# Performance work log

Hardware: AMD Instinct MI355X
Metric: run time of the kernel (lower is better)

The kernel has to match this reference:

```python
import jax, jax.numpy as jnp
import numpy as np

D_INNER = 1024
STATE = 16
DT_RANK = 64  # ceil(d_inner / 16)
LOG_EPS = -7.0
CLAMP = 20.0


def setup_inputs() -> dict:
    key = jax.random.key(0)
    ks = jax.random.split(key, 4)
    B, L = 2, 1024
    x = jax.random.normal(ks[0], (B, L, D_INNER), jnp.float32)
    # x_proj: Linear(d_inner -> dt_rank + 2*state_size, bias=False); stored as (in, out)
    W_xproj = jax.random.normal(ks[1], (D_INNER, DT_RANK + 2 * STATE), jnp.float32) * 0.02
    # dt_proj: Linear(dt_rank -> d_inner, bias=True)
    W_dt = jax.random.normal(ks[2], (DT_RANK, D_INNER), jnp.float32) * 0.02
    b_dt = jax.random.normal(ks[3], (D_INNER,), jnp.float32) * 0.02
    # A_log = log(arange(1..state_size)) repeated over d_inner rows
    A_log = jnp.log(jnp.tile(jnp.arange(1, STATE + 1, dtype=jnp.float32), (D_INNER, 1)))
    D = jnp.ones((D_INNER,), jnp.float32)
    return {"x": x, "W_xproj": W_xproj, "W_dt": W_dt, "b_dt": b_dt, "A_log": A_log, "D": D}


def reference(x, W_xproj, W_dt, b_dt, A_log, D):
    # x: (B, L, d_inner)
    proj = x @ W_xproj  # (B, L, dt_rank + 2*N)
    dt_inter = proj[..., :DT_RANK]
    B_ssm = proj[..., DT_RANK:DT_RANK + STATE]   # (B, L, N)
    C_ssm = proj[..., DT_RANK + STATE:]          # (B, L, N)

    delta = jax.nn.softplus(dt_inter @ W_dt + b_dt)  # (B, L, d_inner)

    # discretization (ZOH)
    A = -jnp.exp(A_log)  # (d_inner, N), negative
    log_delta_A = jnp.clip(delta[..., None] * A[None, None], LOG_EPS, CLAMP)
    delta_A = jnp.exp(log_delta_A)                              # (B, L, d, N)
    delta_B_u = (delta[..., None] * B_ssm[:, :, None, :]) * x[..., None]  # (B, L, d, N)

    # log-space cumsum scan
    log_dA = jnp.log(jnp.clip(delta_A, 1e-7, None))
    log_R = jnp.cumsum(log_dA, axis=1)
    R = jnp.exp(jnp.minimum(log_R, CLAMP))
    exp_neg_log_R = jnp.exp(jnp.minimum(-log_R, CLAMP))
    S = jnp.cumsum(delta_B_u * exp_neg_log_R, axis=1)
    h = R * S  # (B, L, d, N)

    y = jnp.einsum('bln,bldn->bld', C_ssm, h) + x * D
    return y
```

## Files before the change

kernel.cpp:

```cpp
#include <hip/hip_runtime.h>
#include <math.h>

#define D_INNER 1024
#define STATE   16
#define DT_RANK 64
#define NPROJ   96
#define LSEQ    1024
#define NBATCH  2

#define LOG2E   1.4426950408889634f
#define NEG7L2  (-7.0f * LOG2E)
#define P20L2   (20.0f * LOG2E)

template<int CTRL, int RMASK>
__device__ __forceinline__ float dppadd(float v) {
    int t = __builtin_amdgcn_update_dpp(0, __float_as_int(v), CTRL, RMASK, 0xf, false);
    return v + __int_as_float(t);
}
__device__ __forceinline__ float wave_iscan(float v) {
    v = dppadd<0x111, 0xf>(v);
    v = dppadd<0x112, 0xf>(v);
    v = dppadd<0x114, 0xf>(v);
    v = dppadd<0x118, 0xf>(v);
    v = dppadd<0x142, 0xa>(v);
    v = dppadd<0x143, 0xc>(v);
    return v;
}

__global__ __launch_bounds__(768) void proj_kernel(
        const float* __restrict__ x, const float* __restrict__ Wx,
        float* __restrict__ projdt, float* __restrict__ Bg, float* __restrict__ Cg) {
    const int tid = threadIdx.x;
    const int j  = tid % 96;
    const int kq = tid / 96;
    const int row0 = blockIdx.x * 8;

    __shared__ float xs[8 * 1024];
    __shared__ float red[8][8][96];

    {
        const float4* src = (const float4*)(x + (size_t)row0 * 1024);
        #pragma unroll
        for (int i = 0; i < 3; ++i) {
            int idx = tid + 768 * i;
            if (idx < 2048) {
                float4 v = src[idx];
                *(float4*)&xs[idx * 4] = v;
            }
        }
    }
    __syncthreads();

    const float* wp = Wx + (size_t)(kq * 128) * 96 + j;
    const float* xk = &xs[kq * 128];

    float a[8];
    #pragma unroll
    for (int r = 0; r < 8; ++r) a[r] = 0.f;

    #pragma unroll 8
    for (int k = 0; k < 128; ++k) {
        float w = wp[(size_t)k * 96];
        #pragma unroll
        for (int r = 0; r < 8; ++r)
            a[r] = fmaf(xk[r * 1024 + k], w, a[r]);
    }

    #pragma unroll
    for (int r = 0; r < 8; ++r) red[kq][r][j] = a[r];
    __syncthreads();

    {
        const int r  = tid / 96;
        const int jj = tid % 96;
        float s = 0.f;
        #pragma unroll
        for (int p = 0; p < 8; ++p) s += red[p][r][jj];
        const int row = row0 + r;
        const int b = row >> 10, l = row & 1023;
        if (jj < 64)      projdt[(size_t)row * 64 + jj] = s;
        else if (jj < 80) Bg[((size_t)b * 16 + (jj - 64)) * 1024 + l] = s;
        else              Cg[((size_t)b * 16 + (jj - 80)) * 1024 + l] = s;
    }
}

__global__ __launch_bounds__(256) void delta_kernel(
        const float* __restrict__ projdt, const float* __restrict__ Wdt,
        const float* __restrict__ bdt, const float* __restrict__ x,
        float* __restrict__ delta_t, float* __restrict__ u_t) {
    const int bid = blockIdx.x;
    const int lt = bid >> 4;
    const int dt = bid & 15;
    const int row0 = lt * 64;
    const int d0 = dt * 64;
    const int tid = threadIdx.x;

    __shared__ float pl[64][69];
    __shared__ float wlbuf[64 * 68];
    __shared__ float dtile[64][65];
    float (*wl)[68] = (float(*)[68])wlbuf;

    {
        const float4* src = (const float4*)(projdt + (size_t)row0 * 64);
        #pragma unroll
        for (int i = 0; i < 4; ++i) {
            int f4i = tid + 256 * i;
            float4 v = src[f4i];
            int l = f4i >> 4, k4 = (f4i & 15) << 2;
            pl[l][k4+0] = v.x; pl[l][k4+1] = v.y; pl[l][k4+2] = v.z; pl[l][k4+3] = v.w;
        }
    }
    {
        #pragma unroll
        for (int i = 0; i < 4; ++i) {
            int f4i = tid + 256 * i;
            int k = f4i >> 4, m4 = (f4i & 15) << 2;
            float4 v = *(const float4*)(Wdt + (size_t)k * 1024 + d0 + m4);
            *(float4*)&wl[k][m4] = v;
        }
    }
    __syncthreads();

    const int lsub = tid & 63;
    const int dq = tid >> 6;
    float acc[16];
    #pragma unroll
    for (int i = 0; i < 16; ++i) acc[i] = 0.f;

    #pragma unroll 4
    for (int k = 0; k < 64; ++k) {
        float p = pl[lsub][k];
        const float4* wr = (const float4*)&wl[k][dq * 16];
        float4 w0 = wr[0], w1 = wr[1], w2 = wr[2], w3 = wr[3];
        acc[0]  = fmaf(p, w0.x, acc[0]);  acc[1]  = fmaf(p, w0.y, acc[1]);
        acc[2]  = fmaf(p, w0.z, acc[2]);  acc[3]  = fmaf(p, w0.w, acc[3]);
        acc[4]  = fmaf(p, w1.x, acc[4]);  acc[5]  = fmaf(p, w1.y, acc[5]);
        acc[6]  = fmaf(p, w1.z, acc[6]);  acc[7]  = fmaf(p, w1.w, acc[7]);
        acc[8]  = fmaf(p, w2.x, acc[8]);  acc[9]  = fmaf(p, w2.y, acc[9]);
        acc[10] = fmaf(p, w2.z, acc[10]); acc[11] = fmaf(p, w2.w, acc[11]);
        acc[12] = fmaf(p, w3.x, acc[12]); acc[13] = fmaf(p, w3.y, acc[13]);
        acc[14] = fmaf(p, w3.z, acc[14]); acc[15] = fmaf(p, w3.w, acc[15]);
    }

    #pragma unroll
    for (int i = 0; i < 16; ++i) {
        float v = acc[i] + bdt[d0 + dq * 16 + i];
        float sp = fmaxf(v, 0.f) + log1pf(__expf(-fabsf(v)));
        dtile[dq * 16 + i][lsub] = sp;
    }
    __syncthreads();

    float (*xs)[65] = (float(*)[65])wlbuf;
    {
        #pragma unroll
        for (int i = 0; i < 4; ++i) {
            int f4i = tid + 256 * i;
            int l = f4i >> 4, m4 = (f4i & 15) << 2;
            float4 v = *(const float4*)(x + (size_t)(row0 + l) * 1024 + d0 + m4);
            xs[l][m4+0] = v.x; xs[l][m4+1] = v.y; xs[l][m4+2] = v.z; xs[l][m4+3] = v.w;
        }
    }
    __syncthreads();

    {
        int dp_ = tid >> 2, seg = tid & 3;
        int b = row0 >> 10, l0 = row0 & 1023;
        size_t off = ((size_t)b * 1024 + d0 + dp_) * 1024 + l0 + seg * 16;
        float* ddst = delta_t + off;
        float* udst = u_t + off;
        #pragma unroll
        for (int m = 0; m < 4; ++m) {
            int lb = seg * 16 + m * 4;
            float4 v;
            v.x = dtile[dp_][lb + 0];
            v.y = dtile[dp_][lb + 1];
            v.z = dtile[dp_][lb + 2];
            v.w = dtile[dp_][lb + 3];
            float4 u;
            u.x = v.x * xs[lb + 0][dp_];
            u.y = v.y * xs[lb + 1][dp_];
            u.z = v.z * xs[lb + 2][dp_];
            u.w = v.w * xs[lb + 3][dp_];
            ((float4*)ddst)[m] = v;
            ((float4*)udst)[m] = u;
        }
    }
}

__global__ __launch_bounds__(256, 6) void scan_kernel(
        float* delta_m,
        const float* __restrict__ u_t,
        const float* __restrict__ Bg, const float* __restrict__ Cg,
        const float* __restrict__ A_log, const float* __restrict__ Dvec) {
    const int bid0 = blockIdx.x;
    const int bid  = (bid0 & 7) * 256 + (bid0 >> 3);
    const int b = bid >> 10;
    const int d = bid & 1023;
    const int lane = threadIdx.x & 63;
    const int q = threadIdx.x >> 6;
    const int l0 = q * 256 + lane * 4;

    __shared__ float tot1[4][4];
    __shared__ float tot2[4][4];

    const size_t choff = ((size_t)b * 1024 + d) * 1024 + l0;
    const float4 d4 = *(const float4*)(delta_m + choff);
    const float4 u4 = *(const float4*)(u_t + choff);
    const float* Bp = Bg + (size_t)b * 16 * 1024 + l0;
    const float* Cp = Cg + (size_t)b * 16 * 1024 + l0;

    const float Dd = Dvec[d];
    float y0 = u4.x * __builtin_amdgcn_rcpf(d4.x) * Dd;
    float y1 = u4.y * __builtin_amdgcn_rcpf(d4.y) * Dd;
    float y2 = u4.z * __builtin_amdgcn_rcpf(d4.z) * Dd;
    float y3 = u4.w * __builtin_amdgcn_rcpf(d4.w) * Dd;

    #pragma unroll 1
    for (int g = 0; g < 4; ++g) {
        float A2[4], coff[4];
        #pragma unroll
        for (int j = 0; j < 4; ++j)
            A2[j] = -__expf(A_log[d * 16 + g * 4 + j]) * LOG2E;

        #pragma unroll
        for (int j = 0; j < 4; ++j) {
            float a = A2[j];
            float local = fmaxf(d4.x * a, NEG7L2) + fmaxf(d4.y * a, NEG7L2)
                        + fmaxf(d4.z * a, NEG7L2) + fmaxf(d4.w * a, NEG7L2);
            float incl = wave_iscan(local);
            if (lane == 63) tot1[j][q] = incl;
            coff[j] = incl - local;
        }
        __syncthreads();
        #pragma unroll
        for (int j = 0; j < 4; ++j) {
            float4 t = *(const float4*)&tot1[j][0];
            float w = 0.f;
            w += (q > 0) ? t.x : 0.f;
            w += (q > 1) ? t.y : 0.f;
            w += (q > 2) ? t.z : 0.f;
            coff[j] += w;
        }

        float G[4][4];
        #pragma unroll
        for (int j = 0; j < 4; ++j) {
            float a = A2[j];
            float4 bv = *(const float4*)(Bp + (size_t)(g * 4 + j) * 1024);
            float4 cv = *(const float4*)(Cp + (size_t)(g * 4 + j) * 1024);
            float c = coff[j];

            c += fmaxf(d4.x * a, NEG7L2);
            float g0 = cv.x * exp2f(c);
            float srun = u4.x * bv.x * exp2f(fminf(-c, P20L2));
            y0 = fmaf(g0, srun, y0);

            c += fmaxf(d4.y * a, NEG7L2);
            float g1 = cv.y * exp2f(c);
            srun = fmaf(u4.y * bv.y, exp2f(fminf(-c, P20L2)), srun);
            y1 = fmaf(g1, srun, y1);

            c += fmaxf(d4.z * a, NEG7L2);
            float g2 = cv.z * exp2f(c);
            srun = fmaf(u4.z * bv.z, exp2f(fminf(-c, P20L2)), srun);
            y2 = fmaf(g2, srun, y2);

            c += fmaxf(d4.w * a, NEG7L2);
            float g3 = cv.w * exp2f(c);
            srun = fmaf(u4.w * bv.w, exp2f(fminf(-c, P20L2)), srun);
            y3 = fmaf(g3, srun, y3);

            float incl = wave_iscan(srun);
            if (lane == 63) tot2[j][q] = incl;
            float lex = incl - srun;
            y0 = fmaf(g0, lex, y0);
            y1 = fmaf(g1, lex, y1);
            y2 = fmaf(g2, lex, y2);
            y3 = fmaf(g3, lex, y3);
            G[j][0] = g0; G[j][1] = g1; G[j][2] = g2; G[j][3] = g3;
        }
        __syncthreads();
        #pragma unroll
        for (int j = 0; j < 4; ++j) {
            float4 t = *(const float4*)&tot2[j][0];
            float w = 0.f;
            w += (q > 0) ? t.x : 0.f;
            w += (q > 1) ? t.y : 0.f;
            w += (q > 2) ? t.z : 0.f;
            y0 = fmaf(G[j][0], w, y0);
            y1 = fmaf(G[j][1], w, y1);
            y2 = fmaf(G[j][2], w, y2);
            y3 = fmaf(G[j][3], w, y3);
        }
    }

    *(float4*)(delta_m + choff) = make_float4(y0, y1, y2, y3);
}

__global__ __launch_bounds__(256) void finish_kernel(
        const float* __restrict__ M, float* __restrict__ y) {
    const int bid = blockIdx.x;
    const int b  = bid >> 8;
    const int t  = bid & 255;
    const int tl = t >> 4;
    const int td = t & 15;
    const int tid = threadIdx.x;

    __shared__ float T[64][65];

    const float* Mb = M + (size_t)b * 1024 * 1024;
    float* yb = y + (size_t)b * 1024 * 1024;

    #pragma unroll
    for (int i = 0; i < 4; ++i) {
        int fi = tid + 256 * i;
        int r = fi >> 4, c4 = (fi & 15) << 2;
        float4 v = *(const float4*)(Mb + (size_t)(td * 64 + r) * 1024 + tl * 64 + c4);
        T[r][c4+0] = v.x; T[r][c4+1] = v.y; T[r][c4+2] = v.z; T[r][c4+3] = v.w;
    }
    __syncthreads();

    #pragma unroll
    for (int i = 0; i < 4; ++i) {
        int fi = tid + 256 * i;
        int r = fi >> 4, c4 = (fi & 15) << 2;
        float4 o;
        o.x = T[c4+0][r];
        o.y = T[c4+1][r];
        o.z = T[c4+2][r];
        o.w = T[c4+3][r];
        *(float4*)(yb + (size_t)(tl * 64 + r) * 1024 + td * 64 + c4) = o;
    }
}

extern "C" void kernel_launch(void* const* d_in, const int* in_sizes, int n_in,
                              void* d_out, int out_size, void* d_ws, size_t ws_size,
                              hipStream_t stream) {
    const float* x    = (const float*)d_in[0];
    const float* Wx   = (const float*)d_in[1];
    const float* Wdt  = (const float*)d_in[2];
    const float* bdt  = (const float*)d_in[3];
    const float* Alog = (const float*)d_in[4];
    const float* Dvec = (const float*)d_in[5];
    float* y = (float*)d_out;

    float* projdt  = (float*)d_ws;
    float* Bgp     = projdt + (size_t)2048 * 64;
    float* Cgp     = Bgp + (size_t)2 * 16 * 1024;
    float* delta_t = Cgp + (size_t)2 * 16 * 1024;
    float* u_t     = delta_t + (size_t)2 * 1024 * 1024;

    proj_kernel<<<256, 768, 0, stream>>>(x, Wx, projdt, Bgp, Cgp);
    delta_kernel<<<512, 256, 0, stream>>>(projdt, Wdt, bdt, x, delta_t, u_t);
    scan_kernel<<<2048, 256, 0, stream>>>(delta_t, u_t, Bgp, Cgp, Alog, Dvec);
    finish_kernel<<<512, 256, 0, stream>>>(delta_t, y);
}
```

Before: 73.22 us.

## Assign one full scan chain per wavefront, removing cross-wave shared-memory sync

The scan kernel now gives each wavefront a whole (batch, channel) sequence of 1024 steps, with 16 elements per lane, instead of splitting one chain across four waves of a block. This removes the shared-memory totals and the __syncthreads barriers between waves. The grid shrinks from 2048 to 512 blocks and the state loop runs over all 16 states one at a time. In exchange each thread holds many more registers (16-wide delta, u, y, B, C and g arrays), which may lower occupancy, and each lane's strided 64-byte accesses may coalesce less well.

```diff
diff --git a/kernel.cpp b/kernel.cpp
--- a/kernel.cpp
+++ b/kernel.cpp
@@ -187,114 +187,85 @@
     }
 }
 
-__global__ __launch_bounds__(256, 6) void scan_kernel(
+__global__ __launch_bounds__(256) void scan_kernel(
         float* delta_m,
         const float* __restrict__ u_t,
         const float* __restrict__ Bg, const float* __restrict__ Cg,
         const float* __restrict__ A_log, const float* __restrict__ Dvec) {
     const int bid0 = blockIdx.x;
-    const int bid  = (bid0 & 7) * 256 + (bid0 >> 3);
-    const int b = bid >> 10;
-    const int d = bid & 1023;
+    const int bid  = (bid0 & 7) * 64 + (bid0 >> 3);
+    const int w    = threadIdx.x >> 6;
     const int lane = threadIdx.x & 63;
-    const int q = threadIdx.x >> 6;
-    const int l0 = q * 256 + lane * 4;
-
-    __shared__ float tot1[4][4];
-    __shared__ float tot2[4][4];
+    const int chain = bid * 4 + w;
+    const int b = chain >> 10;
+    const int d = chain & 1023;
+    const int l0 = lane * 16;
 
     const size_t choff = ((size_t)b * 1024 + d) * 1024 + l0;
-    const float4 d4 = *(const float4*)(delta_m + choff);
-    const float4 u4 = *(const float4*)(u_t + choff);
+
+    float dl[16], ul[16];
+    #pragma unroll
+    for (int k = 0; k < 4; ++k) {
+        float4 v = *(const float4*)(delta_m + choff + k * 4);
+        dl[4*k+0] = v.x; dl[4*k+1] = v.y; dl[4*k+2] = v.z; dl[4*k+3] = v.w;
+    }
+    #pragma unroll
+    for (int k = 0; k < 4; ++k) {
+        float4 v = *(const float4*)(u_t + choff + k * 4);
+        ul[4*k+0] = v.x; ul[4*k+1] = v.y; ul[4*k+2] = v.z; ul[4*k+3] = v.w;
+    }
+
     const float* Bp = Bg + (size_t)b * 16 * 1024 + l0;
     const float* Cp = Cg + (size_t)b * 16 * 1024 + l0;
-
     const float Dd = Dvec[d];
-    float y0 = u4.x * __builtin_amdgcn_rcpf(d4.x) * Dd;
-    float y1 = u4.y * __builtin_amdgcn_rcpf(d4.y) * Dd;
-    float y2 = u4.z * __builtin_amdgcn_rcpf(d4.z) * Dd;
-    float y3 = u4.w * __builtin_amdgcn_rcpf(d4.w) * Dd;
+
+    float y[16];
+    #pragma unroll
+    for (int l = 0; l < 16; ++l)
+        y[l] = ul[l] * __builtin_amdgcn_rcpf(dl[l]) * Dd;
 
     #pragma unroll 1
-    for (int g = 0; g < 4; ++g) {
-        float A2[4], coff[4];
-        #pragma unroll
-        for (int j = 0; j < 4; ++j)
-            A2[j] = -__expf(A_log[d * 16 + g * 4 + j]) * LOG2E;
-
-        #pragma unroll
-        for (int j = 0; j < 4; ++j) {
-            float a = A2[j];
-            float local = fmaxf(d4.x * a, NEG7L2) + fmaxf(d4.y * a, NEG7L2)
-                        + fmaxf(d4.z * a, NEG7L2) + fmaxf(d4.w * a, NEG7L2);
-            float incl = wave_iscan(local);
-            if (lane == 63) tot1[j][q] = incl;
-            coff[j] = incl - local;
-        }
-        __syncthreads();
-        #pragma unroll
-        for (int j = 0; j < 4; ++j) {
-            float4 t = *(const float4*)&tot1[j][0];
-            float w = 0.f;
-            w += (q > 0) ? t.x : 0.f;
-            w += (q > 1) ? t.y : 0.f;
-            w += (q > 2) ? t.z : 0.f;
-            coff[j] += w;
-        }
-
-        float G[4][4];
-        #pragma unroll
-        for (int j = 0; j < 4; ++j) {
-            float a = A2[j];
-            float4 bv = *(const float4*)(Bp + (size_t)(g * 4 + j) * 1024);
-            float4 cv = *(const float4*)(Cp + (size_t)(g * 4 + j) * 1024);
-            float c = coff[j];
-
-            c += fmaxf(d4.x * a, NEG7L2);
-            float g0 = cv.x * exp2f(c);
-            float srun = u4.x * bv.x * exp2f(fminf(-c, P20L2));
-            y0 = fmaf(g0, srun, y0);
-
-            c += fmaxf(d4.y * a, NEG7L2);
-            float g1 = cv.y * exp2f(c);
-            srun = fmaf(u4.y * bv.y, exp2f(fminf(-c, P20L2)), srun);
-            y1 = fmaf(g1, srun, y1);
-
-            c += fmaxf(d4.z * a, NEG7L2);
-            float g2 = cv.z * exp2f(c);
-            srun = fmaf(u4.z * bv.z, exp2f(fminf(-c, P20L2)), srun);
-            y2 = fmaf(g2, srun, y2);
-
-            c += fmaxf(d4.w * a, NEG7L2);
-            float g3 = cv.w * exp2f(c);
-            srun = fmaf(u4.w * bv.w, exp2f(fminf(-c, P20L2)), srun);
-            y3 = fmaf(g3, srun, y3);
-
-            float incl = wave_iscan(srun);
-            if (lane == 63) tot2[j][q] = incl;
-            float lex = incl - srun;
-            y0 = fmaf(g0, lex, y0);
-            y1 = fmaf(g1, lex, y1);
-            y2 = fmaf(g2, lex, y2);
-            y3 = fmaf(g3, lex, y3);
-            G[j][0] = g0; G[j][1] = g1; G[j][2] = g2; G[j][3] = g3;
-        }
-        __syncthreads();
-        #pragma unroll
-        for (int j = 0; j < 4; ++j) {
-            float4 t = *(const float4*)&tot2[j][0];
-            float w = 0.f;
-            w += (q > 0) ? t.x : 0.f;
-            w += (q > 1) ? t.y : 0.f;
-            w += (q > 2) ? t.z : 0.f;
-            y0 = fmaf(G[j][0], w, y0);
-            y1 = fmaf(G[j][1], w, y1);
-            y2 = fmaf(G[j][2], w, y2);
-            y3 = fmaf(G[j][3], w, y3);
-        }
-    }
-
-    *(float4*)(delta_m + choff) = make_float4(y0, y1, y2, y3);
+    for (int n = 0; n < 16; ++n) {
+        const float a = -__expf(A_log[d * 16 + n]) * LOG2E;
+
+        float local = 0.f;
+        #pragma unroll
+        for (int l = 0; l < 16; ++l)
+            local += fmaxf(dl[l] * a, NEG7L2);
+        float incl = wave_iscan(local);
+        float c = incl - local;
+
+        float Bv[16], Cv[16];
+        #pragma unroll
+        for (int k = 0; k < 4; ++k) {
+            float4 bv = *(const float4*)(Bp + (size_t)n * 1024 + k * 4);
+            Bv[4*k+0] = bv.x; Bv[4*k+1] = bv.y; Bv[4*k+2] = bv.z; Bv[4*k+3] = bv.w;
+            float4 cv = *(const float4*)(Cp + (size_t)n * 1024 + k * 4);
+            Cv[4*k+0] = cv.x; Cv[4*k+1] = cv.y; Cv[4*k+2] = cv.z; Cv[4*k+3] = cv.w;
+        }
+
+        float g[16];
+        float srun = 0.f;
+        #pragma unroll
+        for (int l = 0; l < 16; ++l) {
+            c += fmaxf(dl[l] * a, NEG7L2);
+            g[l] = Cv[l] * exp2f(c);
+            srun = fmaf(ul[l] * Bv[l], exp2f(fminf(-c, P20L2)), srun);
+            y[l] = fmaf(g[l], srun, y[l]);
+        }
+
+        float incl2 = wave_iscan(srun);
+        float lex = incl2 - srun;
+        #pragma unroll
+        for (int l = 0; l < 16; ++l)
+            y[l] = fmaf(g[l], lex, y[l]);
+    }
+
+    #pragma unroll
+    for (int k = 0; k < 4; ++k) {
+        float4 o = make_float4(y[4*k+0], y[4*k+1], y[4*k+2], y[4*k+3]);
+        *(float4*)(delta_m + choff + k * 4) = o;
+    }
 }
 
 __global__ __launch_bounds__(256) void finish_kernel(
@@ -352,6 +323,6 @@
 
     proj_kernel<<<256, 768, 0, stream>>>(x, Wx, projdt, Bgp, Cgp);
     delta_kernel<<<512, 256, 0, stream>>>(projdt, Wdt, bdt, x, delta_t, u_t);
-    scan_kernel<<<2048, 256, 0, stream>>>(delta_t, u_t, Bgp, Cgp, Alog, Dvec);
+    scan_kernel<<<512, 256, 0, stream>>>(delta_t, u_t, Bgp, Cgp, Alog, Dvec);
     finish_kernel<<<512, 256, 0, stream>>>(delta_t, y);
 }
```

Measured after the change: 71.15 us. 1.03x faster.
